# Kernel tuning notes

Measured on AMD Instinct MI355X. Metric: run time of the kernel, lower is better.

Reference implementation:

```python
import jax, jax.numpy as jnp
from jax import lax
import numpy as np

B, T, V, E, H = 2048, 512, 4, 64, 128


def setup_inputs() -> dict:
    key = jax.random.key(0)
    ks = jax.random.split(key, 8)
    s = 0.1  # small init scale
    x = jax.random.randint(ks[0], (B, T), 0, V, dtype=jnp.int64)
    emb = jax.random.normal(ks[1], (V, E), dtype=jnp.float32) * s
    W_ih = jax.random.normal(ks[2], (3 * H, E), dtype=jnp.float32) * s
    W_hh = jax.random.normal(ks[3], (3 * H, H), dtype=jnp.float32) * s
    b_ih = jax.random.normal(ks[4], (3 * H,), dtype=jnp.float32) * s
    b_hh = jax.random.normal(ks[5], (3 * H,), dtype=jnp.float32) * s
    W_fc = jax.random.normal(ks[6], (V, H), dtype=jnp.float32) * s
    b_fc = jax.random.normal(ks[7], (V,), dtype=jnp.float32) * s
    return {"x": x, "emb": emb, "W_ih": W_ih, "W_hh": W_hh,
            "b_ih": b_ih, "b_hh": b_hh, "W_fc": W_fc, "b_fc": b_fc}


def reference(x, emb, W_ih, W_hh, b_ih, b_hh, W_fc, b_fc):
    # Embedding lookup: [B, T, E]
    xe = emb[x]
    # Precompute all input-side gate projections in one big GEMM: [B, T, 3H]
    gi = jnp.einsum("bte,ge->btg", xe, W_ih) + b_ih
    gi = jnp.swapaxes(gi, 0, 1)  # [T, B, 3H] for scan over time

    def step(h, gi_t):
        # PyTorch GRU gate order: r, z, n
        gi_r, gi_z, gi_n = jnp.split(gi_t, 3, axis=-1)
        gh = h @ W_hh.T + b_hh  # [B, 3H]
        gh_r, gh_z, gh_n = jnp.split(gh, 3, axis=-1)
        r = jax.nn.sigmoid(gi_r + gh_r)
        z = jax.nn.sigmoid(gi_z + gh_z)
        n = jnp.tanh(gi_n + r * gh_n)
        h_new = (1.0 - z) * n + z * h
        return h_new, None

    h0 = jnp.zeros((x.shape[0], H), dtype=gi.dtype)
    hT, _ = lax.scan(step, h0, gi)  # only final hidden state is needed
    logits = hT @ W_fc.T + b_fc  # [B, V]
    return logits
```

## Files before the change

kernel.cpp:

```cpp
#include <hip/hip_runtime.h>
#include <hip/hip_bf16.h>


#define B_  2048
#define T_  512
#define V_  4
#define E_  64
#define H_  128
#define G3  384
#define G3P 392
#define SH  136
#define NB  8

#define LOG2E 1.4426950408889634f

typedef __attribute__((ext_vector_type(8))) short  short8;
typedef __attribute__((ext_vector_type(4))) float  float4v;
typedef __attribute__((ext_vector_type(2))) float  f32x2;

__device__ __forceinline__ short bf16s(float f) {
  union { float ff; unsigned int u; } c; c.ff = f;
  return (short)((c.u + 0x7fffu + ((c.u >> 16) & 1u)) >> 16);
}

__global__ void gi_table_kernel(const float* __restrict__ emb,
                                const float* __restrict__ W_ih,
                                const float* __restrict__ b_ih,
                                const float* __restrict__ b_hh,
                                float* __restrict__ table) {
  int gid = blockIdx.x * blockDim.x + threadIdx.x;
  if (gid >= V_ * G3) return;
  int v = gid / G3;
  int g = gid - v * G3;
  float acc = b_ih[g];
  if (g < 2 * H_) acc += b_hh[g];
  const float* wr = W_ih + g * E_;
  const float* er = emb + v * E_;
#pragma unroll 8
  for (int e = 0; e < E_; ++e) acc += wr[e] * er[e];
  table[gid] = acc * ((g < 2 * H_) ? -LOG2E : 2.f * LOG2E);
}

#define MFMA16(A, B, C) __builtin_amdgcn_mfma_f32_16x16x32_bf16((A), (B), (C), 0, 0, 0)

__global__ __launch_bounds__(512) void gru_kernel(
    const int* __restrict__ x, const float* __restrict__ W_hh,
    const float* __restrict__ b_hh, const float* __restrict__ W_fc,
    const float* __restrict__ b_fc, const float* __restrict__ table,
    float* __restrict__ out) {
  __shared__ __align__(16) short hbuf[2][16 * SH];
  __shared__ __align__(16) unsigned char xs[(T_ + 2) * NB];
  __shared__ __align__(16) float tabS[V_ * G3P];
  __shared__ __align__(16) float hf[NB * H_];

  const int tid  = threadIdx.x;
  const int w    = tid >> 6;
  const int lane = tid & 63;
  const int m    = lane & 15;
  const int q    = lane >> 4;
  const int mb   = m & 7;
  const bool isHi = (m & 8) != 0;
  const int g0   = blockIdx.x * NB;

  for (int i = tid; i < NB * T_; i += 512) {
    int r = i >> 9;
    int t = i & (T_ - 1);
    xs[t * NB + r] = (unsigned char)(x[(g0 + r) * T_ + t] & 3);
  }
  if (tid < 16) xs[T_ * NB + tid] = 0;
  for (int v = 0; v < V_; ++v)
    for (int g = tid; g < G3; g += 512) tabS[v * G3P + g] = table[v * G3 + g];
  for (int i = tid; i < 2 * 16 * SH; i += 512) hbuf[0][i] = 0;

  short8 wA[3][4];
#pragma unroll
  for (int s = 0; s < 3; ++s) {
    const float sc = (s < 2) ? -LOG2E : 2.f * LOG2E;
    const float* wrow = W_hh + (s * H_ + w * 16 + m) * H_;
#pragma unroll
    for (int ks = 0; ks < 4; ++ks) {
      const float* p = wrow + ks * 32 + q * 8;
      short8 f;
#pragma unroll
      for (int jj = 0; jj < 8; ++jj) f[jj] = bf16s(p[jj] * sc);
      wA[s][ks] = f;
    }
  }

  const int c0  = w * 16 + q * 4;
  const int c0r = c0 + (isHi ? 2 : 0);
  float4v bhnC;
  {
    const float* p = b_hh + 2 * H_ + c0;
#pragma unroll
    for (int i = 0; i < 4; ++i) bhnC[i] = p[i] * 2.f * LOG2E;
  }
  f32x2 hA = {0.f, 0.f};

  __syncthreads();

  float4v gAR, gAZ, gBR, gBZ;
  f32x2 gAN, gBN;
  int vb;
  {
    int v0 = xs[mb] & 3;
    const float* tb = &tabS[v0 * G3P + c0];
    gAR = *(const float4v*)(tb);
    gAZ = *(const float4v*)(tb + H_);
    gAN = *(const f32x2*)(&tabS[v0 * G3P + 2 * H_ + c0r]);
    vb  = xs[NB + mb];
  }

  const f32x2 one2 = {1.f, 1.f};

  auto sel = [&](const float4v& xv) -> f32x2 {
    f32x2 r;
    r.x = isHi ? xv[2] : xv[0];
    r.y = isHi ? xv[3] : xv[1];
    return r;
  };

  auto step = [&](int FROM, int TO, int t,
                  float4v& guR, float4v& guZ, f32x2& guN,
                  float4v& glR, float4v& glZ, f32x2& glN) {
    const short* rbp = &hbuf[FROM][m * SH + q * 8];
    short8 h0 = *(const short8*)(rbp);
    short8 h1 = *(const short8*)(rbp + 32);
    short8 h2 = *(const short8*)(rbp + 64);
    short8 h3 = *(const short8*)(rbp + 96);

    float4v a0 = MFMA16(wA[0][0], h0, guR);
    a0 = MFMA16(wA[0][1], h1, a0);
    a0 = MFMA16(wA[0][2], h2, a0);
    a0 = MFMA16(wA[0][3], h3, a0);
    float4v a2 = MFMA16(wA[2][0], h0, bhnC);
    a2 = MFMA16(wA[2][1], h1, a2);
    a2 = MFMA16(wA[2][2], h2, a2);
    a2 = MFMA16(wA[2][3], h3, a2);
    float4v a1 = MFMA16(wA[1][0], h0, guZ);
    a1 = MFMA16(wA[1][1], h1, a1);
    a1 = MFMA16(wA[1][2], h2, a1);
    a1 = MFMA16(wA[1][3], h3, a1);

    f32x2 a0e = sel(a0);
    f32x2 rr;
    rr.x = __builtin_amdgcn_rcpf(1.f + __builtin_amdgcn_exp2f(a0e.x));
    rr.y = __builtin_amdgcn_rcpf(1.f + __builtin_amdgcn_exp2f(a0e.y));
    f32x2 a2e = sel(a2);
    f32x2 a1e = sel(a1);

    int vb2 = xs[(t + 2) * NB + mb];
    const float* tbn = &tabS[(vb & 3) * G3P + c0];
    glR = *(const float4v*)(tbn);
    glZ = *(const float4v*)(tbn + H_);
    glN = *(const f32x2*)(tbn + 2 * H_ + (isHi ? 2 : 0));
    vb = vb2;

    f32x2 np = rr * a2e + guN;
    f32x2 e  = {__builtin_amdgcn_exp2f(np.x), __builtin_amdgcn_exp2f(np.y)};
    f32x2 Ez = {__builtin_amdgcn_exp2f(a1e.x), __builtin_amdgcn_exp2f(a1e.y)};
    f32x2 num = e * (Ez + hA) + (hA - Ez);
    f32x2 den = (e + one2) * (one2 + Ez);
    f32x2 rc  = {__builtin_amdgcn_rcpf(den.x), __builtin_amdgcn_rcpf(den.y)};
    hA = num * rc;
    unsigned int pk0;
    asm("v_cvt_pk_bf16_f32 %0, %1, %2" : "=v"(pk0) : "v"(hA.x), "v"(hA.y));
    *(unsigned int*)(&hbuf[TO][mb * SH + c0r]) = pk0;
    *(unsigned int*)(&hbuf[TO][(mb + 8) * SH + c0r]) = pk0;
    __syncthreads();
  };

  for (int t = 0; t < T_; t += 2) {
    step(0, 1, t,     gAR, gAZ, gAN, gBR, gBZ, gBN);
    step(1, 0, t + 1, gBR, gBZ, gBN, gAR, gAZ, gAN);
  }

  hf[mb * H_ + c0r + 0] = hA.x;
  hf[mb * H_ + c0r + 1] = hA.y;
  __syncthreads();

  if (tid < 32) {
    int row = tid >> 2, vo = tid & 3;
    float s = b_fc[vo];
    const float* wv = W_fc + vo * H_;
    const float* hr = &hf[row * H_];
#pragma unroll 4
    for (int k = 0; k < H_; k += 4)
      s += hr[k] * wv[k] + hr[k + 1] * wv[k + 1]
         + hr[k + 2] * wv[k + 2] + hr[k + 3] * wv[k + 3];
    out[(g0 + row) * V_ + vo] = s;
  }
}

extern "C" void kernel_launch(void* const* d_in, const int* in_sizes, int n_in,
                              void* d_out, int out_size, void* d_ws, size_t ws_size,
                              hipStream_t stream) {
  const int*   x    = (const int*)d_in[0];
  const float* emb  = (const float*)d_in[1];
  const float* W_ih = (const float*)d_in[2];
  const float* W_hh = (const float*)d_in[3];
  const float* b_ih = (const float*)d_in[4];
  const float* b_hh = (const float*)d_in[5];
  const float* W_fc = (const float*)d_in[6];
  const float* b_fc = (const float*)d_in[7];
  float* out   = (float*)d_out;
  float* table = (float*)d_ws;

  gi_table_kernel<<<(V_ * G3 + 255) / 256, 256, 0, stream>>>(emb, W_ih, b_ih, b_hh, table);
  gru_kernel<<<B_ / NB, 512, 0, stream>>>(x, W_hh, b_hh, W_fc, b_fc, table, out);
}
```

Measured before the change: 285.3 us.

## Halve batch rows per block to four with 4x MFMA row replication

Reduces the number of sequences per workgroup from 8 to 4, doubling the grid to 512 blocks. The 16 MFMA rows now hold 4 copies of each sequence, so each lane handles one hidden element instead of two and the per-step elementwise gate math and LDS writes shrink per lane. The aim is to shorten the serial per-step critical path and spread the work over more CUs. The cost is twice as many blocks and twice the total MFMA work, each running all 512 sequential steps.

```diff
diff --git a/kernel.cpp b/kernel.cpp
--- a/kernel.cpp
+++ b/kernel.cpp
@@ -9,14 +9,13 @@
 #define H_  128
 #define G3  384
 #define G3P 392
-#define SH  136
-#define NB  8
+#define SH  132
+#define NB  4
 
 #define LOG2E 1.4426950408889634f
 
 typedef __attribute__((ext_vector_type(8))) short  short8;
 typedef __attribute__((ext_vector_type(4))) float  float4v;
-typedef __attribute__((ext_vector_type(2))) float  f32x2;
 
 __device__ __forceinline__ short bf16s(float f) {
   union { float ff; unsigned int u; } c; c.ff = f;
@@ -48,7 +47,7 @@
     const float* __restrict__ b_hh, const float* __restrict__ W_fc,
     const float* __restrict__ b_fc, const float* __restrict__ table,
     float* __restrict__ out) {
-  __shared__ __align__(16) short hbuf[2][16 * SH];
+  __shared__ __align__(16) short hbuf[2][NB * SH];
   __shared__ __align__(16) unsigned char xs[(T_ + 2) * NB];
   __shared__ __align__(16) float tabS[V_ * G3P];
   __shared__ __align__(16) float hf[NB * H_];
@@ -58,8 +57,10 @@
   const int lane = tid & 63;
   const int m    = lane & 15;
   const int q    = lane >> 4;
-  const int mb   = m & 7;
-  const bool isHi = (m & 8) != 0;
+  const int mb   = m & 3;
+  const int rep  = m >> 2;
+  const bool rb0 = (m & 4) != 0;
+  const bool rb1 = (m & 8) != 0;
   const int g0   = blockIdx.x * NB;
 
   for (int i = tid; i < NB * T_; i += 512) {
@@ -67,10 +68,10 @@
     int t = i & (T_ - 1);
     xs[t * NB + r] = (unsigned char)(x[(g0 + r) * T_ + t] & 3);
   }
-  if (tid < 16) xs[T_ * NB + tid] = 0;
+  if (tid < 2 * NB) xs[T_ * NB + tid] = 0;
   for (int v = 0; v < V_; ++v)
     for (int g = tid; g < G3; g += 512) tabS[v * G3P + g] = table[v * G3 + g];
-  for (int i = tid; i < 2 * 16 * SH; i += 512) hbuf[0][i] = 0;
+  for (int i = tid; i < 2 * NB * SH; i += 512) hbuf[0][i] = 0;
 
   short8 wA[3][4];
 #pragma unroll
@@ -88,42 +89,39 @@
   }
 
   const int c0  = w * 16 + q * 4;
-  const int c0r = c0 + (isHi ? 2 : 0);
+  const int c0r = c0 + rep;
   float4v bhnC;
   {
     const float* p = b_hh + 2 * H_ + c0;
 #pragma unroll
     for (int i = 0; i < 4; ++i) bhnC[i] = p[i] * 2.f * LOG2E;
   }
-  f32x2 hA = {0.f, 0.f};
+  float h = 0.f;
 
   __syncthreads();
 
   float4v gAR, gAZ, gBR, gBZ;
-  f32x2 gAN, gBN;
+  float gAN, gBN;
   int vb;
   {
     int v0 = xs[mb] & 3;
     const float* tb = &tabS[v0 * G3P + c0];
     gAR = *(const float4v*)(tb);
     gAZ = *(const float4v*)(tb + H_);
-    gAN = *(const f32x2*)(&tabS[v0 * G3P + 2 * H_ + c0r]);
+    gAN = tabS[v0 * G3P + 2 * H_ + c0r];
     vb  = xs[NB + mb];
   }
 
-  const f32x2 one2 = {1.f, 1.f};
-
-  auto sel = [&](const float4v& xv) -> f32x2 {
-    f32x2 r;
-    r.x = isHi ? xv[2] : xv[0];
-    r.y = isHi ? xv[3] : xv[1];
-    return r;
+  auto sel = [&](const float4v& xv) -> float {
+    float lo = rb0 ? xv[1] : xv[0];
+    float hi = rb0 ? xv[3] : xv[2];
+    return rb1 ? hi : lo;
   };
 
   auto step = [&](int FROM, int TO, int t,
-                  float4v& guR, float4v& guZ, f32x2& guN,
-                  float4v& glR, float4v& glZ, f32x2& glN) {
-    const short* rbp = &hbuf[FROM][m * SH + q * 8];
+                  float4v& guR, float4v& guZ, float& guN,
+                  float4v& glR, float4v& glZ, float& glN) {
+    const short* rbp = &hbuf[FROM][mb * SH + q * 8];
     short8 h0 = *(const short8*)(rbp);
     short8 h1 = *(const short8*)(rbp + 32);
     short8 h2 = *(const short8*)(rbp + 64);
@@ -142,31 +140,27 @@
     a1 = MFMA16(wA[1][2], h2, a1);
     a1 = MFMA16(wA[1][3], h3, a1);
 
-    f32x2 a0e = sel(a0);
-    f32x2 rr;
-    rr.x = __builtin_amdgcn_rcpf(1.f + __builtin_amdgcn_exp2f(a0e.x));
-    rr.y = __builtin_amdgcn_rcpf(1.f + __builtin_amdgcn_exp2f(a0e.y));
-    f32x2 a2e = sel(a2);
-    f32x2 a1e = sel(a1);
+    float a0e = sel(a0);
+    float rr  = __builtin_amdgcn_rcpf(1.f + __builtin_amdgcn_exp2f(a0e));
+    float a2e = sel(a2);
+    float a1e = sel(a1);
 
     int vb2 = xs[(t + 2) * NB + mb];
     const float* tbn = &tabS[(vb & 3) * G3P + c0];
     glR = *(const float4v*)(tbn);
     glZ = *(const float4v*)(tbn + H_);
-    glN = *(const f32x2*)(tbn + 2 * H_ + (isHi ? 2 : 0));
+    glN = tbn[2 * H_ + rep];
     vb = vb2;
 
-    f32x2 np = rr * a2e + guN;
-    f32x2 e  = {__builtin_amdgcn_exp2f(np.x), __builtin_amdgcn_exp2f(np.y)};
-    f32x2 Ez = {__builtin_amdgcn_exp2f(a1e.x), __builtin_amdgcn_exp2f(a1e.y)};
-    f32x2 num = e * (Ez + hA) + (hA - Ez);
-    f32x2 den = (e + one2) * (one2 + Ez);
-    f32x2 rc  = {__builtin_amdgcn_rcpf(den.x), __builtin_amdgcn_rcpf(den.y)};
-    hA = num * rc;
-    unsigned int pk0;
-    asm("v_cvt_pk_bf16_f32 %0, %1, %2" : "=v"(pk0) : "v"(hA.x), "v"(hA.y));
-    *(unsigned int*)(&hbuf[TO][mb * SH + c0r]) = pk0;
-    *(unsigned int*)(&hbuf[TO][(mb + 8) * SH + c0r]) = pk0;
+    float np  = rr * a2e + guN;
+    float e   = __builtin_amdgcn_exp2f(np);
+    float Ez  = __builtin_amdgcn_exp2f(a1e);
+    float num = e * (Ez + h) + (h - Ez);
+    float den = (e + 1.f) * (1.f + Ez);
+    h = num * __builtin_amdgcn_rcpf(den);
+    unsigned int pk;
+    asm("v_cvt_pk_bf16_f32 %0, %1, %2" : "=v"(pk) : "v"(h), "v"(h));
+    *(unsigned short*)(&hbuf[TO][mb * SH + c0r]) = (unsigned short)pk;
     __syncthreads();
   };
 
@@ -175,11 +169,10 @@
     step(1, 0, t + 1, gBR, gBZ, gBN, gAR, gAZ, gAN);
   }
 
-  hf[mb * H_ + c0r + 0] = hA.x;
-  hf[mb * H_ + c0r + 1] = hA.y;
+  hf[mb * H_ + c0r] = h;
   __syncthreads();
 
-  if (tid < 32) {
+  if (tid < NB * V_) {
     int row = tid >> 2, vo = tid & 3;
     float s = b_fc[vo];
     const float* wv = W_fc + vo * H_;
```

New measurement: 1.075 ms. 277% more time.

## Keep gate input table in registers and select by token instead of LDS loads

Applied to the files above, without the earlier changes.

Loads all four vocabulary rows of the precomputed input-gate table into registers once, then picks the current token's row with conditional selects each step instead of reading LDS. Tokens are stored row-major per batch and fetched eight at a time as a 64-bit word, the loop is unrolled by eight, the duplicate hidden-state write for MFMA rows 8-15 is dropped (both halves now read the same 8 rows), and launch bounds ask for two blocks per CU. The aim is fewer LDS accesses and less latency on the serial recurrence, at the cost of more VGPRs and select instructions, which could hurt occupancy under the tighter register budget.

```diff
diff --git a/kernel.cpp b/kernel.cpp
--- a/kernel.cpp
+++ b/kernel.cpp
@@ -11,12 +11,14 @@
 #define G3P 392
 #define SH  136
 #define NB  8
+#define TP  528
 
 #define LOG2E 1.4426950408889634f
 
 typedef __attribute__((ext_vector_type(8))) short  short8;
 typedef __attribute__((ext_vector_type(4))) float  float4v;
 typedef __attribute__((ext_vector_type(2))) float  f32x2;
+typedef unsigned long long ull;
 
 __device__ __forceinline__ short bf16s(float f) {
   union { float ff; unsigned int u; } c; c.ff = f;
@@ -43,13 +45,13 @@
 
 #define MFMA16(A, B, C) __builtin_amdgcn_mfma_f32_16x16x32_bf16((A), (B), (C), 0, 0, 0)
 
-__global__ __launch_bounds__(512) void gru_kernel(
+__global__ __launch_bounds__(512, 2) void gru_kernel(
     const int* __restrict__ x, const float* __restrict__ W_hh,
     const float* __restrict__ b_hh, const float* __restrict__ W_fc,
     const float* __restrict__ b_fc, const float* __restrict__ table,
     float* __restrict__ out) {
-  __shared__ __align__(16) short hbuf[2][16 * SH];
-  __shared__ __align__(16) unsigned char xs[(T_ + 2) * NB];
+  __shared__ __align__(16) short hbuf[2][NB * SH];
+  __shared__ __align__(16) unsigned char xs2[NB * TP];
   __shared__ __align__(16) float tabS[V_ * G3P];
   __shared__ __align__(16) float hf[NB * H_];
 
@@ -65,12 +67,15 @@
   for (int i = tid; i < NB * T_; i += 512) {
     int r = i >> 9;
     int t = i & (T_ - 1);
-    xs[t * NB + r] = (unsigned char)(x[(g0 + r) * T_ + t] & 3);
-  }
-  if (tid < 16) xs[T_ * NB + tid] = 0;
+    xs2[r * TP + t] = (unsigned char)(x[(g0 + r) * T_ + t] & 3);
+  }
+  if (tid < NB * 16) {
+    int r = tid >> 4, k = tid & 15;
+    xs2[r * TP + T_ + k] = 0;
+  }
   for (int v = 0; v < V_; ++v)
     for (int g = tid; g < G3; g += 512) tabS[v * G3P + g] = table[v * G3 + g];
-  for (int i = tid; i < 2 * 16 * SH; i += 512) hbuf[0][i] = 0;
+  for (int i = tid; i < 2 * NB * SH; i += 512) hbuf[0][i] = 0;
 
   short8 wA[3][4];
 #pragma unroll
@@ -99,16 +104,39 @@
 
   __syncthreads();
 
+  float4v gRv[4], gZv[4];
+  f32x2   gNv[4];
+#pragma unroll
+  for (int v = 0; v < 4; ++v) {
+    const float* tb = &tabS[v * G3P + c0];
+    gRv[v] = *(const float4v*)(tb);
+    gZv[v] = *(const float4v*)(tb + H_);
+    gNv[v] = *(const f32x2*)(tb + 2 * H_ + (isHi ? 2 : 0));
+  }
+
+  ull cur8 = *(const ull*)&xs2[mb * TP];
+
+  auto pickf = [&](unsigned tk, float a, float b, float c, float d) -> float {
+    float lo = (tk & 1u) ? b : a;
+    float hi = (tk & 1u) ? d : c;
+    return (tk & 2u) ? hi : lo;
+  };
+  auto pick4 = [&](unsigned tk, const float4v& a, const float4v& b,
+                   const float4v& c, const float4v& d) -> float4v {
+    float4v r;
+#pragma unroll
+    for (int i = 0; i < 4; ++i) r[i] = pickf(tk, a[i], b[i], c[i], d[i]);
+    return r;
+  };
+
   float4v gAR, gAZ, gBR, gBZ;
   f32x2 gAN, gBN;
-  int vb;
   {
-    int v0 = xs[mb] & 3;
-    const float* tb = &tabS[v0 * G3P + c0];
-    gAR = *(const float4v*)(tb);
-    gAZ = *(const float4v*)(tb + H_);
-    gAN = *(const f32x2*)(&tabS[v0 * G3P + 2 * H_ + c0r]);
-    vb  = xs[NB + mb];
+    unsigned tk = (unsigned)(cur8 & 3ull);
+    gAR = pick4(tk, gRv[0], gRv[1], gRv[2], gRv[3]);
+    gAZ = pick4(tk, gZv[0], gZv[1], gZv[2], gZv[3]);
+    gAN.x = pickf(tk, gNv[0].x, gNv[1].x, gNv[2].x, gNv[3].x);
+    gAN.y = pickf(tk, gNv[0].y, gNv[1].y, gNv[2].y, gNv[3].y);
   }
 
   const f32x2 one2 = {1.f, 1.f};
@@ -120,10 +148,10 @@
     return r;
   };
 
-  auto step = [&](int FROM, int TO, int t,
+  auto step = [&](int FROM, int TO, unsigned tk,
                   float4v& guR, float4v& guZ, f32x2& guN,
                   float4v& glR, float4v& glZ, f32x2& glN) {
-    const short* rbp = &hbuf[FROM][m * SH + q * 8];
+    const short* rbp = &hbuf[FROM][mb * SH + q * 8];
     short8 h0 = *(const short8*)(rbp);
     short8 h1 = *(const short8*)(rbp + 32);
     short8 h2 = *(const short8*)(rbp + 64);
@@ -149,12 +177,10 @@
     f32x2 a2e = sel(a2);
     f32x2 a1e = sel(a1);
 
-    int vb2 = xs[(t + 2) * NB + mb];
-    const float* tbn = &tabS[(vb & 3) * G3P + c0];
-    glR = *(const float4v*)(tbn);
-    glZ = *(const float4v*)(tbn + H_);
-    glN = *(const f32x2*)(tbn + 2 * H_ + (isHi ? 2 : 0));
-    vb = vb2;
+    glR = pick4(tk, gRv[0], gRv[1], gRv[2], gRv[3]);
+    glZ = pick4(tk, gZv[0], gZv[1], gZv[2], gZv[3]);
+    glN.x = pickf(tk, gNv[0].x, gNv[1].x, gNv[2].x, gNv[3].x);
+    glN.y = pickf(tk, gNv[0].y, gNv[1].y, gNv[2].y, gNv[3].y);
 
     f32x2 np = rr * a2e + guN;
     f32x2 e  = {__builtin_amdgcn_exp2f(np.x), __builtin_amdgcn_exp2f(np.y)};
@@ -166,20 +192,25 @@
     unsigned int pk0;
     asm("v_cvt_pk_bf16_f32 %0, %1, %2" : "=v"(pk0) : "v"(hA.x), "v"(hA.y));
     *(unsigned int*)(&hbuf[TO][mb * SH + c0r]) = pk0;
-    *(unsigned int*)(&hbuf[TO][(mb + 8) * SH + c0r]) = pk0;
     __syncthreads();
   };
 
-  for (int t = 0; t < T_; t += 2) {
-    step(0, 1, t,     gAR, gAZ, gAN, gBR, gBZ, gBN);
-    step(1, 0, t + 1, gBR, gBZ, gBN, gAR, gAZ, gAN);
+  for (int t = 0; t < T_; t += 8) {
+    ull nxt8 = *(const ull*)&xs2[mb * TP + t + 8];
+#pragma unroll
+    for (int p = 0; p < 8; ++p) {
+      unsigned tk = (unsigned)(((p + 1) < 8 ? (cur8 >> ((p + 1) * 8)) : nxt8) & 3ull);
+      if ((p & 1) == 0) step(0, 1, tk, gAR, gAZ, gAN, gBR, gBZ, gBN);
+      else              step(1, 0, tk, gBR, gBZ, gBN, gAR, gAZ, gAN);
+    }
+    cur8 = nxt8;
   }
 
   hf[mb * H_ + c0r + 0] = hA.x;
   hf[mb * H_ + c0r + 1] = hA.y;
   __syncthreads();
 
-  if (tid < 32) {
+  if (tid < NB * V_) {
     int row = tid >> 2, vo = tid & 3;
     float s = b_fc[vo];
     const float* wv = W_fc + vo * H_;
```

New measurement: 324.2 us. +13.7%, slower.
